# Kernel tuning notes

Measured on AMD Instinct MI355X. Metric: run time of the kernel, lower is better.

## Reference

```python
import jax, jax.numpy as jnp
import numpy as np

B, S, D = 16, 2048, 400
HEADS, HEAD_SIZE = 4, 100
SCALE = 1.0 / np.float32(100.0 ** 0.5)


def setup_inputs() -> dict:
    key = jax.random.key(0)
    ks = jax.random.split(key, 8)
    return {
        "x": jax.random.normal(ks[0], (B, S, D), jnp.float32),
        "attn_kernel": jax.random.normal(ks[1], (3, D, HEAD_SIZE), jnp.float32) * 0.05,
        "attn_dense": jax.random.normal(ks[2], (D, HEADS * HEAD_SIZE), jnp.float32) * 0.05,
        "d1_w": jax.random.normal(ks[3], (400, 400), jnp.float32) * 0.05,
        "d1_b": jnp.zeros((400,), jnp.float32),
        "fc1_w": jax.random.normal(ks[4], (800, 512), jnp.float32) * 0.05,
        "fc1_b": jnp.zeros((512,), jnp.float32),
        "fc2_w": jax.random.normal(ks[5], (512, 256), jnp.float32) * 0.05,
        "fc2_b": jnp.zeros((256,), jnp.float32),
    }


def reference(x, attn_kernel, attn_dense, d1_w, d1_b, fc1_w, fc1_b, fc2_w, fc2_b):
    # Multi-head attention. NOTE: the original loops `heads` times over the SAME
    # shared kernel, so all 4 head outputs are identical; compute once, tile.
    WQ = jnp.einsum('bsd,dh->bsh', x, attn_kernel[0])  # [B,S,100]
    WK = jnp.einsum('bsd,dh->bsh', x, attn_kernel[1])
    WV = jnp.einsum('bsd,dh->bsh', x, attn_kernel[2])
    scores = jnp.einsum('bqh,bkh->bqk', WQ, WK) * SCALE  # [B,S,S]
    probs = jax.nn.softmax(scores, axis=-1)
    V = jnp.einsum('bqk,bkh->bqh', probs, WV)  # [B,S,100]
    out = jnp.tile(V, (1, 1, HEADS))  # concat of identical heads -> [B,S,400]
    out = jnp.einsum('bsd,de->bse', out, attn_dense)  # [B,S,400]
    # Dropout layers are identity at inference.
    h = jax.nn.relu(jnp.einsum('bsd,de->bse', out, d1_w) + d1_b)  # [B,S,400]
    pooled = jnp.concatenate([jnp.max(h, axis=1), jnp.mean(h, axis=1)], axis=-1)  # [B,800]
    h = jax.nn.relu(pooled @ fc1_w + fc1_b)  # [B,512]
    h = jax.nn.relu(h @ fc2_w + fc2_b)  # [B,256]
    return h
```

## Files before the change

kernel.cpp:

```cpp
#include <hip/hip_runtime.h>

typedef __attribute__((ext_vector_type(8))) _Float16 f16x8;
typedef __attribute__((ext_vector_type(4))) float f4v;
typedef __attribute__((ext_vector_type(8))) unsigned short us8;
typedef __attribute__((ext_vector_type(4))) unsigned short us4;
typedef unsigned short u16;

__device__ __forceinline__ u16 h2b(_Float16 h) { return __builtin_bit_cast(u16, h); }
__device__ __forceinline__ float b2f(u16 b) {
    return (float)__builtin_bit_cast(_Float16, b);
}

#define BAR() do { asm volatile("s_waitcnt lgkmcnt(0)" ::: "memory"); \
                   __builtin_amdgcn_s_barrier(); } while (0)

__global__ void k_w2p(const float* __restrict__ ad, const float* __restrict__ d1w,
                      float* __restrict__ w2p) {
    int i = blockIdx.x * 256 + threadIdx.x;
    if (i >= 51200) return;
    int es = blockIdx.y;
    int d = i / 400, j = i % 400;
    float acc = 0.f;
    if (d < 100) {
        const float* a0 = ad + d * 400 + es * 100;
        const float* wr = d1w + (es * 100) * 400 + j;
        #pragma unroll 4
        for (int e = 0; e < 100; ++e) {
            float av = a0[e] + a0[40000 + e] + a0[80000 + e] + a0[120000 + e];
            acc += av * wr[e * 400];
        }
    }
    w2p[es * 51200 + i] = acc;
}

__global__ void k_w2r(const float* __restrict__ w2p, u16* __restrict__ w2f) {
    int i = blockIdx.x * 256 + threadIdx.x;
    if (i >= 51200) return;
    float acc = w2p[i] + w2p[51200 + i] + w2p[102400 + i] + w2p[153600 + i];
    int d = i / 400, j = i % 400;
    int idx = ((j >> 4) * 4 + (d >> 5)) * 512 + (((d >> 3) & 3) * 16 + (j & 15)) * 8 + (d & 7);
    w2f[idx] = h2b((_Float16)acc);
}

__global__ void k_wprep(const float* __restrict__ ak, u16* __restrict__ wsp) {
    int i = blockIdx.x * 256 + threadIdx.x;
    if (i >= 159744) return;
    int k = i & 31, n = (i >> 5) & 127;
    int xx = i >> 12;
    int ks = xx % 13, m = xx / 13;
    int gk = ks * 32 + k;
    float v = (n < 100 && gk < 400) ? ak[m * 40000 + gk * 100 + n] : 0.f;
    _Float16 hb = (_Float16)v;
    _Float16 lb = (_Float16)(v - (float)hb);
    long base = (long)xx * 8192;
    int pos = n * 32 + ((((k >> 3) ^ (n & 3)) << 3) | (k & 7));
    wsp[base + pos] = h2b(hb);
    wsp[base + 4096 + pos] = h2b(lb);
}

__global__ __launch_bounds__(512) void k_gemm_qkv(
    const float* __restrict__ x, const u16* __restrict__ wsp,
    u16* __restrict__ QH, u16* __restrict__ KH, u16* __restrict__ VT) {
    __shared__ __align__(16) u16 smem[32768];

    const int tid = threadIdx.x;
    const int bx = blockIdx.x;
    const int m = bx % 3;
    const int rowblk = bx / 3;
    const long row0 = (long)rowblk * 128;
    const int w = tid >> 6, l = tid & 63, g = l >> 4, c15 = l & 15;
    const int sr = tid >> 2, skc = tid & 3;

    f4v acc[8];
    #pragma unroll
    for (int nt = 0; nt < 8; ++nt) acc[nt] = (f4v){0.f, 0.f, 0.f, 0.f};

    const u16* wbase = wsp + (long)m * 13 * 8192;
    float4 xr0, xr1;
    us8 wr[2];
    const int xpos = sr * 32 + ((skc * 8) ^ ((sr & 3) << 3));

    {
        const float* xp = x + (row0 + sr) * 400 + skc * 8;
        xr0 = *(const float4*)xp;
        xr1 = *(const float4*)(xp + 4);
        #pragma unroll
        for (int r = 0; r < 2; ++r)
            wr[r] = *(const us8*)&wbase[(long)(tid + r * 512) * 8];
        float va[8] = {xr0.x, xr0.y, xr0.z, xr0.w, xr1.x, xr1.y, xr1.z, xr1.w};
        us8 hi8, lo8;
        #pragma unroll
        for (int j = 0; j < 8; ++j) {
            _Float16 h = (_Float16)va[j];
            hi8[j] = h2b(h);
            lo8[j] = h2b((_Float16)(va[j] - (float)h));
        }
        *(us8*)&smem[xpos] = hi8;
        *(us8*)&smem[4096 + xpos] = lo8;
        #pragma unroll
        for (int r = 0; r < 2; ++r) {
            int u = tid + r * 512;
            *(us8*)&smem[8192 + (u >> 9) * 4096 + (u & 511) * 8] = wr[r];
        }
        const float* xp1 = x + (row0 + sr) * 400 + 32 + skc * 8;
        xr0 = *(const float4*)xp1;
        xr1 = *(const float4*)(xp1 + 4);
        const u16* wsrc = wbase + 8192;
        #pragma unroll
        for (int r = 0; r < 2; ++r)
            wr[r] = *(const us8*)&wsrc[(long)(tid + r * 512) * 8];
    }

    for (int ks = 0; ks < 13; ++ks) {
        BAR();
        u16* cb = smem + (ks & 1) * 16384;
        u16* sb = smem + ((ks & 1) ^ 1) * 16384;
        if (ks + 1 < 13) {
            float va[8] = {xr0.x, xr0.y, xr0.z, xr0.w, xr1.x, xr1.y, xr1.z, xr1.w};
            us8 hi8, lo8;
            #pragma unroll
            for (int j = 0; j < 8; ++j) {
                _Float16 h = (_Float16)va[j];
                hi8[j] = h2b(h);
                lo8[j] = h2b((_Float16)(va[j] - (float)h));
            }
            *(us8*)&sb[xpos] = hi8;
            *(us8*)&sb[4096 + xpos] = lo8;
            #pragma unroll
            for (int r = 0; r < 2; ++r) {
                int u = tid + r * 512;
                *(us8*)&sb[8192 + (u >> 9) * 4096 + (u & 511) * 8] = wr[r];
            }
            if (ks + 2 < 13) {
                if ((ks + 2) * 32 + skc * 8 < 400) {
                    const float* xp = x + (row0 + sr) * 400 + (ks + 2) * 32 + skc * 8;
                    xr0 = *(const float4*)xp;
                    xr1 = *(const float4*)(xp + 4);
                } else {
                    xr0 = make_float4(0.f, 0.f, 0.f, 0.f);
                    xr1 = make_float4(0.f, 0.f, 0.f, 0.f);
                }
                const u16* wsrc = wbase + (long)(ks + 2) * 8192;
                #pragma unroll
                for (int r = 0; r < 2; ++r)
                    wr[r] = *(const us8*)&wsrc[(long)(tid + r * 512) * 8];
            }
        }
        const int arow = w * 16 + c15;
        const int axo = arow * 32 + ((g * 8) ^ ((arow & 3) << 3));
        f16x8 ah = *(const f16x8*)&cb[axo];
        f16x8 al = *(const f16x8*)&cb[4096 + axo];
        __builtin_amdgcn_s_setprio(1);
        #pragma unroll
        for (int nt = 0; nt < 8; ++nt) {
            int brow = nt * 16 + c15;
            int boff = brow * 32 + ((g * 8) ^ ((brow & 3) << 3));
            f16x8 bh = *(const f16x8*)&cb[8192 + boff];
            acc[nt] = __builtin_amdgcn_mfma_f32_16x16x32_f16(ah, bh, acc[nt], 0, 0, 0);
            acc[nt] = __builtin_amdgcn_mfma_f32_16x16x32_f16(al, bh, acc[nt], 0, 0, 0);
            if (m != 2) {
                f16x8 bl = *(const f16x8*)&cb[12288 + boff];
                acc[nt] = __builtin_amdgcn_mfma_f32_16x16x32_f16(ah, bl, acc[nt], 0, 0, 0);
            }
        }
        __builtin_amdgcn_s_setprio(0);
    }
    BAR();
    u16* epi = smem;

    if (m == 2) {
        const int q0 = w * 16 + 4 * g;
        const int vtile = q0 >> 6, q0w = q0 & 63;
        #pragma unroll
        for (int nt = 0; nt < 8; ++nt) {
            int d = nt * 16 + c15;
            if (d < 112) {
                us4 v4;
                #pragma unroll
                for (int r = 0; r < 4; ++r) v4[r] = h2b((_Float16)acc[nt][r]);
                *(us4*)&epi[vtile * 8192 + d * 64 + (q0w ^ ((d & 7) << 3))] = v4;
            }
        }
        __syncthreads();
        #pragma unroll
        for (int r = 0; r < 4; ++r) {
            int u = tid + r * 512;
            int vt2 = u >> 10, uu = u & 1023;
            if (uu < 896)
                *(us8*)&VT[((long)(2 * rowblk + vt2)) * 8192 + (long)uu * 8] =
                    *(const us8*)&epi[u * 8];
        }
    } else {
        const float qs = (m == 0) ? 0.14426950408889634f : 1.0f;
        #pragma unroll
        for (int nt = 0; nt < 8; ++nt) {
            #pragma unroll
            for (int r = 0; r < 4; ++r) {
                int row = w * 16 + 4 * g + r, col = nt * 16 + c15;
                epi[row * 128 + (col ^ ((row & 7) << 3))] =
                    h2b((_Float16)(acc[nt][r] * qs));
            }
        }
        __syncthreads();
        if (m == 0) {
            #pragma unroll
            for (int r = 0; r < 4; ++r) {
                int u = tid + r * 512;
                int row = u >> 4, c = u & 15;
                *(us8*)&QH[(row0 + row) * 128 + c * 8] =
                    *(const us8*)&epi[row * 128 + ((c * 8) ^ ((row & 7) << 3))];
            }
        } else {
            u16* dst = KH + (long)rowblk * 16384;
            #pragma unroll
            for (int r = 0; r < 4; ++r) {
                int u = tid + r * 512;
                *(us8*)&dst[(long)u * 8] = *(const us8*)&epi[u * 8];
            }
        }
    }
}

__global__ __launch_bounds__(512) void k_flash(
    const u16* __restrict__ Qg, const u16* __restrict__ Kg,
    const u16* __restrict__ Vg, u16* __restrict__ VOI,
    float* __restrict__ ML) {
    __shared__ __align__(16) char KS[2][16384];
    __shared__ __align__(16) char VS[2][14336];
    __shared__ __align__(16) char PS[8][2048];

    const int tid = threadIdx.x;
    const int w = tid >> 6, l = tid & 63, g = l >> 4, c15 = l & 15;
    const int b = blockIdx.y, qt = blockIdx.x, half = blockIdx.z;
    const int t0 = half * 16;

    const u16* qp = Qg + ((long)b * 2048 + qt * 128 + w * 16 + c15) * 128;
    f16x8 qh[4];
    #pragma unroll
    for (int ks = 0; ks < 4; ++ks) qh[ks] = *(const f16x8*)(qp + ks * 32 + g * 8);

    f4v O[7];
    #pragma unroll
    for (int i = 0; i < 7; ++i) O[i] = (f4v){0.f, 0.f, 0.f, 0.f};
    float lrow = 0.f;

    const u16* Kb = Kg + (long)b * 32 * 8192;
    const u16* Vb = Vg + (long)b * 32 * 8192;
    char* Pw = PS[w];

    us8 kreg[2], vreg[2];
    #pragma unroll
    for (int r = 0; r < 2; ++r) {
        int u = tid + r * 512;
        kreg[r] = *(const us8*)(Kb + (long)t0 * 8192 + (long)u * 8);
        if (u < 896) vreg[r] = *(const us8*)(Vb + (long)t0 * 8192 + (long)u * 8);
    }
    #pragma unroll
    for (int r = 0; r < 2; ++r) {
        int u = tid + r * 512;
        *(us8*)(KS[0] + u * 16) = kreg[r];
        if (u < 896) *(us8*)(VS[0] + u * 16) = vreg[r];
    }
    #pragma unroll
    for (int r = 0; r < 2; ++r) {
        int u = tid + r * 512;
        kreg[r] = *(const us8*)(Kb + (long)(t0 + 1) * 8192 + (long)u * 8);
        if (u < 896) vreg[r] = *(const us8*)(Vb + (long)(t0 + 1) * 8192 + (long)u * 8);
    }

    for (int t = t0; t < t0 + 16; ++t) {
        const int cur = (t - t0) & 1;
        BAR();
        if (t + 1 < t0 + 16) {
            #pragma unroll
            for (int r = 0; r < 2; ++r) {
                int u = tid + r * 512;
                *(us8*)(KS[cur ^ 1] + u * 16) = kreg[r];
                if (u < 896) *(us8*)(VS[cur ^ 1] + u * 16) = vreg[r];
            }
            if (t + 2 < t0 + 16) {
                #pragma unroll
                for (int r = 0; r < 2; ++r) {
                    int u = tid + r * 512;
                    kreg[r] = *(const us8*)(Kb + (long)(t + 2) * 8192 + (long)u * 8);
                    if (u < 896)
                        vreg[r] = *(const us8*)(Vb + (long)(t + 2) * 8192 + (long)u * 8);
                }
            }
        }
        const char* Kc = KS[cur];
        const char* Vc = VS[cur];

        f4v s[4];
        #pragma unroll
        for (int nt = 0; nt < 4; ++nt) s[nt] = (f4v){0.f, 0.f, 0.f, 0.f};
        __builtin_amdgcn_s_setprio(1);
        #pragma unroll
        for (int ks = 0; ks < 4; ++ks) {
            #pragma unroll
            for (int nt = 0; nt < 4; ++nt) {
                int key = nt * 16 + c15;
                f16x8 kf = *(const f16x8*)(Kc + key * 256 +
                                           ((ks * 64 + g * 16) ^ ((key & 7) << 4)));
                s[nt] = __builtin_amdgcn_mfma_f32_16x16x32_f16(kf, qh[ks], s[nt], 0, 0, 0);
            }
        }
        __builtin_amdgcn_s_setprio(0);

        float sum = 0.f;
        #pragma unroll
        for (int nt = 0; nt < 4; ++nt) {
            #pragma unroll
            for (int r = 0; r < 4; ++r) {
                float p = exp2f(s[nt][r]);
                s[nt][r] = p;
                sum += p;
            }
        }
        sum += __shfl_xor(sum, 16);
        sum += __shfl_xor(sum, 32);
        lrow += sum;

        #pragma unroll
        for (int nt = 0; nt < 4; ++nt) {
            uint2 pw2;
            pw2.x = __builtin_bit_cast(unsigned int,
                        __builtin_amdgcn_cvt_pkrtz(s[nt][0], s[nt][1]));
            pw2.y = __builtin_bit_cast(unsigned int,
                        __builtin_amdgcn_cvt_pkrtz(s[nt][2], s[nt][3]));
            *(uint2*)(Pw + c15 * 128 + ((32 * nt + 8 * g) ^ ((c15 & 7) << 4))) = pw2;
        }
        __builtin_amdgcn_s_setprio(1);
        #pragma unroll
        for (int k0 = 0; k0 < 2; ++k0) {
            f16x8 pa = *(const f16x8*)(Pw + c15 * 128 +
                                       ((k0 * 64 + g * 16) ^ ((c15 & 7) << 4)));
            #pragma unroll
            for (int dt = 0; dt < 7; ++dt) {
                int d = dt * 16 + c15;
                f16x8 vf = *(const f16x8*)(Vc + d * 128 +
                                           ((k0 * 64 + g * 16) ^ ((d & 7) << 4)));
                O[dt] = __builtin_amdgcn_mfma_f32_16x16x32_f16(pa, vf, O[dt], 0, 0, 0);
            }
        }
        __builtin_amdgcn_s_setprio(0);
    }

    if (g == 0) {
        ((float*)Pw)[c15] = lrow;
        ML[half * 32768 + b * 2048 + qt * 128 + w * 16 + c15] = lrow;
    }
    float linv[4];
    #pragma unroll
    for (int r = 0; r < 4; ++r) linv[r] = 1.f / ((float*)Pw)[4 * g + r];
    u16* vout = VOI + (long)half * 4194304 + ((long)b * 16 + qt) * 16384;
    #pragma unroll
    for (int r = 0; r < 4; ++r) {
        int rowl = w * 16 + 4 * g + r;
        int rsw = (4 * g + r) & 7;
        #pragma unroll
        for (int dt = 0; dt < 7; ++dt) {
            int d = dt * 16 + c15;
            int pos = rowl * 128 + ((((d >> 3) ^ rsw) << 3) | (d & 7));
            vout[pos] = h2b((_Float16)(O[dt][r] * linv[r]));
        }
    }
}

__global__ __launch_bounds__(256) void k_hpool(
    const u16* __restrict__ VOI, const float* __restrict__ ML,
    const u16* __restrict__ W2F, const float* __restrict__ d1b,
    float* __restrict__ pmax, float* __restrict__ psum) {
    __shared__ __align__(16) u16 A[8192];
    __shared__ float redM[4][400], redS[4][400];
    __shared__ float wgt[64][2];
    const int tid = threadIdx.x;
    const int w = tid >> 6, l = tid & 63, g = l >> 4, c15 = l & 15;
    const int b = blockIdx.y, rt = blockIdx.x;

    if (tid < 64) {
        float a = ML[b * 2048 + rt * 64 + tid];
        float c = ML[32768 + b * 2048 + rt * 64 + tid];
        float inv = 1.f / (a + c);
        wgt[tid][0] = a * inv;
        wgt[tid][1] = c * inv;
    }
    __syncthreads();

    const u16* s1 = VOI + ((long)b * 32 + rt) * 8192;
    const u16* s2 = s1 + 4194304;
    #pragma unroll
    for (int r = 0; r < 4; ++r) {
        int u = tid + r * 256;
        int row = u >> 4;
        us8 p1 = *(const us8*)&s1[(long)u * 8];
        us8 p2 = *(const us8*)&s2[(long)u * 8];
        float w1 = wgt[row][0], w2 = wgt[row][1];
        us8 o;
        #pragma unroll
        for (int j = 0; j < 8; ++j)
            o[j] = h2b((_Float16)(w1 * b2f(p1[j]) + w2 * b2f(p2[j])));
        *(us8*)&A[u * 8] = o;
    }
    __syncthreads();

    const int arow = w * 16 + c15;
    f16x8 af[4];
    #pragma unroll
    for (int ks = 0; ks < 4; ++ks)
        af[ks] = *(const f16x8*)&A[arow * 128 + ((ks * 32 + g * 8) ^ ((arow & 7) << 3))];

    for (int nt = 0; nt < 25; ++nt) {
        f4v acc = (f4v){0.f, 0.f, 0.f, 0.f};
        #pragma unroll
        for (int ks = 0; ks < 4; ++ks) {
            f16x8 bf = *(const f16x8*)&W2F[(nt * 4 + ks) * 512 + l * 8];
            acc = __builtin_amdgcn_mfma_f32_16x16x32_f16(af[ks], bf, acc, 0, 0, 0);
        }
        float bias = d1b[nt * 16 + c15];
        float mx4 = -1e30f, sm4 = 0.f;
        #pragma unroll
        for (int r = 0; r < 4; ++r) {
            float h = fmaxf(acc[r] + bias, 0.f);
            mx4 = fmaxf(mx4, h);
            sm4 += h;
        }
        mx4 = fmaxf(mx4, __shfl_xor(mx4, 16));
        mx4 = fmaxf(mx4, __shfl_xor(mx4, 32));
        sm4 += __shfl_xor(sm4, 16);
        sm4 += __shfl_xor(sm4, 32);
        if (g == 0) {
            redM[w][nt * 16 + c15] = mx4;
            redS[w][nt * 16 + c15] = sm4;
        }
    }
    __syncthreads();
    for (int j = tid; j < 400; j += 256) {
        float mx = fmaxf(fmaxf(redM[0][j], redM[1][j]), fmaxf(redM[2][j], redM[3][j]));
        float sm = redS[0][j] + redS[1][j] + redS[2][j] + redS[3][j];
        pmax[((long)b * 32 + rt) * 400 + j] = mx;
        psum[((long)b * 32 + rt) * 400 + j] = sm;
    }
}

__global__ __launch_bounds__(256) void k_pred(
    const float* __restrict__ pmax, const float* __restrict__ psum,
    float* __restrict__ pooled) {
    __shared__ float rm[16][17], rs[16][17];
    const int b = blockIdx.x, jt = blockIdx.y, tid = threadIdx.x;
    const int jo = tid & 15, ts = tid >> 4;
    const int j = jt * 16 + jo;
    float mx = -1e30f, sm = 0.f;
    for (int t = ts; t < 32; t += 16) {
        mx = fmaxf(mx, pmax[((long)b * 32 + t) * 400 + j]);
        sm += psum[((long)b * 32 + t) * 400 + j];
    }
    rm[ts][jo] = mx; rs[ts][jo] = sm;
    __syncthreads();
    if (tid < 16) {
        float m2 = rm[0][tid], s2 = rs[0][tid];
        #pragma unroll
        for (int t = 1; t < 16; ++t) { m2 = fmaxf(m2, rm[t][tid]); s2 += rs[t][tid]; }
        pooled[b * 800 + jt * 16 + tid] = m2;
        pooled[b * 800 + 400 + jt * 16 + tid] = s2 * (1.f / 2048.f);
    }
}

__global__ __launch_bounds__(256) void k_fc1(
    const float* __restrict__ pooled, const float* __restrict__ w,
    const float* __restrict__ bias, float* __restrict__ out) {
    __shared__ float pl[800];
    __shared__ float red[16][17];
    const int b = blockIdx.x, jt = blockIdx.y, tid = threadIdx.x;
    const int jo = tid & 15, ks = tid >> 4;
    const int j = jt * 16 + jo;
    for (int i = tid; i < 800; i += 256) pl[i] = pooled[b * 800 + i];
    __syncthreads();
    float acc = 0.f;
    #pragma unroll 5
    for (int kk = 0; kk < 50; ++kk) {
        int k = ks * 50 + kk;
        acc += pl[k] * w[k * 512 + j];
    }
    red[ks][jo] = acc;
    __syncthreads();
    if (tid < 16) {
        float s = red[0][tid];
        #pragma unroll
        for (int t = 1; t < 16; ++t) s += red[t][tid];
        out[b * 512 + jt * 16 + tid] = fmaxf(s + bias[jt * 16 + tid], 0.f);
    }
}

__global__ __launch_bounds__(256) void k_fc2(
    const float* __restrict__ h, const float* __restrict__ w,
    const float* __restrict__ bias, float* __restrict__ out) {
    __shared__ float hl[512];
    __shared__ float red[16][17];
    const int b = blockIdx.x, jt = blockIdx.y, tid = threadIdx.x;
    const int jo = tid & 15, ks = tid >> 4;
    const int j = jt * 16 + jo;
    for (int i = tid; i < 512; i += 256) hl[i] = h[b * 512 + i];
    __syncthreads();
    float acc = 0.f;
    #pragma unroll 4
    for (int kk = 0; kk < 32; ++kk) {
        int k = ks * 32 + kk;
        acc += hl[k] * w[k * 256 + j];
    }
    red[ks][jo] = acc;
    __syncthreads();
    if (tid < 16) {
        float s = red[0][tid];
        #pragma unroll
        for (int t = 1; t < 16; ++t) s += red[t][tid];
        out[b * 256 + jt * 16 + tid] = fmaxf(s + bias[jt * 16 + tid], 0.f);
    }
}

extern "C" void kernel_launch(void* const* d_in, const int* in_sizes, int n_in,
                              void* d_out, int out_size, void* d_ws, size_t ws_size,
                              hipStream_t stream) {
    const float* x          = (const float*)d_in[0];
    const float* attn_kernel= (const float*)d_in[1];
    const float* attn_dense = (const float*)d_in[2];
    const float* d1_w       = (const float*)d_in[3];
    const float* d1_b       = (const float*)d_in[4];
    const float* fc1_w      = (const float*)d_in[5];
    const float* fc1_b      = (const float*)d_in[6];
    const float* fc2_w      = (const float*)d_in[7];
    const float* fc2_b      = (const float*)d_in[8];
    float* out = (float*)d_out;
    char*  wsb = (char*)d_ws;

    u16*    QH   = (u16*)(wsb);
    u16*    KH   = (u16*)(wsb + 8388608);
    u16*    VT   = (u16*)(wsb + 16777216);
    u16*    VOI  = (u16*)(wsb + 25165824);
    u16*    WSP  = (u16*)(wsb + 41943040);
    u16*    W2F  = (u16*)(wsb + 42582016);
    float*  PMAX = (float*)(wsb + 42844416);
    float*  PSUM = (float*)(wsb + 43663616);
    float*  ML   = (float*)(wsb + 44566784);
    float*  W2P  = (float*)(wsb + 44828928);
    float*  POOL = (float*)(wsb + 45648128);
    float*  FC1  = (float*)(wsb + 45699328);

    k_wprep<<<624, 256, 0, stream>>>(attn_kernel, WSP);
    k_w2p <<<dim3(200, 4), 256, 0, stream>>>(attn_dense, d1_w, W2P);
    k_w2r <<<200, 256, 0, stream>>>(W2P, W2F);
    k_gemm_qkv<<<768, 512, 0, stream>>>(x, WSP, QH, KH, VT);
    k_flash<<<dim3(16, 16, 2), 512, 0, stream>>>(QH, KH, VT, VOI, ML);
    k_hpool<<<dim3(32, 16), 256, 0, stream>>>(VOI, ML, W2F, d1_b, PMAX, PSUM);
    k_pred<<<dim3(16, 25), 256, 0, stream>>>(PMAX, PSUM, POOL);
    k_fc1 <<<dim3(16, 32), 256, 0, stream>>>(POOL, fc1_w, fc1_b, FC1);
    k_fc2 <<<dim3(16, 16), 256, 0, stream>>>(FC1, fc2_w, fc2_b, out);
}
```

Before: 153.0 us.

## Fuse Q/K/V projections into one block and double query rows per flash wave

The QKV GEMM now computes Q, K and V for a 128-row tile in a single block, so each x tile is loaded and hi/lo split once instead of three times. The grid shrinks from 768 to 256 blocks and shared memory grows to 96KB. The flash kernel halves its threads to 256 and has each wave process 32 query rows, reusing every K/V fragment read from LDS for two MFMAs. The trade-off is higher register pressure, fewer waves per block, and less occupancy and parallelism in both kernels.

```diff
diff --git a/kernel.cpp b/kernel.cpp
--- a/kernel.cpp
+++ b/kernel.cpp
@@ -61,32 +61,39 @@
 __global__ __launch_bounds__(512) void k_gemm_qkv(
     const float* __restrict__ x, const u16* __restrict__ wsp,
     u16* __restrict__ QH, u16* __restrict__ KH, u16* __restrict__ VT) {
-    __shared__ __align__(16) u16 smem[32768];
+    __shared__ __align__(16) u16 smem[49152];
 
     const int tid = threadIdx.x;
-    const int bx = blockIdx.x;
-    const int m = bx % 3;
-    const int rowblk = bx / 3;
+    const int rowblk = blockIdx.x;
     const long row0 = (long)rowblk * 128;
     const int w = tid >> 6, l = tid & 63, g = l >> 4, c15 = l & 15;
     const int sr = tid >> 2, skc = tid & 3;
 
-    f4v acc[8];
-    #pragma unroll
-    for (int nt = 0; nt < 8; ++nt) acc[nt] = (f4v){0.f, 0.f, 0.f, 0.f};
-
-    const u16* wbase = wsp + (long)m * 13 * 8192;
+    f4v aQ[8], aK[8], aV[8];
+    #pragma unroll
+    for (int nt = 0; nt < 8; ++nt) {
+        aQ[nt] = (f4v){0.f, 0.f, 0.f, 0.f};
+        aK[nt] = (f4v){0.f, 0.f, 0.f, 0.f};
+        aV[nt] = (f4v){0.f, 0.f, 0.f, 0.f};
+    }
+
+    const u16* wq  = wsp;
+    const u16* wkh = wsp + 106496;
+    const u16* wkl = wsp + 110592;
+    const u16* wv  = wsp + 212992;
+
     float4 xr0, xr1;
-    us8 wr[2];
+    us8 wr[4];
     const int xpos = sr * 32 + ((skc * 8) ^ ((sr & 3) << 3));
 
     {
         const float* xp = x + (row0 + sr) * 400 + skc * 8;
         xr0 = *(const float4*)xp;
         xr1 = *(const float4*)(xp + 4);
-        #pragma unroll
-        for (int r = 0; r < 2; ++r)
-            wr[r] = *(const us8*)&wbase[(long)(tid + r * 512) * 8];
+        wr[0] = *(const us8*)&wq [(long)tid * 8];
+        wr[1] = *(const us8*)&wkh[(long)tid * 8];
+        wr[2] = *(const us8*)&wkl[(long)tid * 8];
+        wr[3] = *(const us8*)&wv [(long)tid * 8];
         float va[8] = {xr0.x, xr0.y, xr0.z, xr0.w, xr1.x, xr1.y, xr1.z, xr1.w};
         us8 hi8, lo8;
         #pragma unroll
@@ -97,24 +104,23 @@
         }
         *(us8*)&smem[xpos] = hi8;
         *(us8*)&smem[4096 + xpos] = lo8;
-        #pragma unroll
-        for (int r = 0; r < 2; ++r) {
-            int u = tid + r * 512;
-            *(us8*)&smem[8192 + (u >> 9) * 4096 + (u & 511) * 8] = wr[r];
-        }
+        *(us8*)&smem[8192  + tid * 8] = wr[0];
+        *(us8*)&smem[12288 + tid * 8] = wr[1];
+        *(us8*)&smem[16384 + tid * 8] = wr[2];
+        *(us8*)&smem[20480 + tid * 8] = wr[3];
         const float* xp1 = x + (row0 + sr) * 400 + 32 + skc * 8;
         xr0 = *(const float4*)xp1;
         xr1 = *(const float4*)(xp1 + 4);
-        const u16* wsrc = wbase + 8192;
-        #pragma unroll
-        for (int r = 0; r < 2; ++r)
-            wr[r] = *(const us8*)&wsrc[(long)(tid + r * 512) * 8];
+        wr[0] = *(const us8*)&wq [8192 + (long)tid * 8];
+        wr[1] = *(const us8*)&wkh[8192 + (long)tid * 8];
+        wr[2] = *(const us8*)&wkl[8192 + (long)tid * 8];
+        wr[3] = *(const us8*)&wv [8192 + (long)tid * 8];
     }
 
     for (int ks = 0; ks < 13; ++ks) {
         BAR();
-        u16* cb = smem + (ks & 1) * 16384;
-        u16* sb = smem + ((ks & 1) ^ 1) * 16384;
+        u16* cb = smem + (ks & 1) * 24576;
+        u16* sb = smem + ((ks & 1) ^ 1) * 24576;
         if (ks + 1 < 13) {
             float va[8] = {xr0.x, xr0.y, xr0.z, xr0.w, xr1.x, xr1.y, xr1.z, xr1.w};
             us8 hi8, lo8;
@@ -126,11 +132,10 @@
             }
             *(us8*)&sb[xpos] = hi8;
             *(us8*)&sb[4096 + xpos] = lo8;
-            #pragma unroll
-            for (int r = 0; r < 2; ++r) {
-                int u = tid + r * 512;
-                *(us8*)&sb[8192 + (u >> 9) * 4096 + (u & 511) * 8] = wr[r];
-            }
+            *(us8*)&sb[8192  + tid * 8] = wr[0];
+            *(us8*)&sb[12288 + tid * 8] = wr[1];
+            *(us8*)&sb[16384 + tid * 8] = wr[2];
+            *(us8*)&sb[20480 + tid * 8] = wr[3];
             if (ks + 2 < 13) {
                 if ((ks + 2) * 32 + skc * 8 < 400) {
                     const float* xp = x + (row0 + sr) * 400 + (ks + 2) * 32 + skc * 8;
@@ -140,10 +145,11 @@
                     xr0 = make_float4(0.f, 0.f, 0.f, 0.f);
                     xr1 = make_float4(0.f, 0.f, 0.f, 0.f);
                 }
-                const u16* wsrc = wbase + (long)(ks + 2) * 8192;
-                #pragma unroll
-                for (int r = 0; r < 2; ++r)
-                    wr[r] = *(const us8*)&wsrc[(long)(tid + r * 512) * 8];
+                long wo = (long)(ks + 2) * 8192 + (long)tid * 8;
+                wr[0] = *(const us8*)&wq [wo];
+                wr[1] = *(const us8*)&wkh[wo];
+                wr[2] = *(const us8*)&wkl[wo];
+                wr[3] = *(const us8*)&wv [wo];
             }
         }
         const int arow = w * 16 + c15;
@@ -155,20 +161,63 @@
         for (int nt = 0; nt < 8; ++nt) {
             int brow = nt * 16 + c15;
             int boff = brow * 32 + ((g * 8) ^ ((brow & 3) << 3));
-            f16x8 bh = *(const f16x8*)&cb[8192 + boff];
-            acc[nt] = __builtin_amdgcn_mfma_f32_16x16x32_f16(ah, bh, acc[nt], 0, 0, 0);
-            acc[nt] = __builtin_amdgcn_mfma_f32_16x16x32_f16(al, bh, acc[nt], 0, 0, 0);
-            if (m != 2) {
-                f16x8 bl = *(const f16x8*)&cb[12288 + boff];
-                acc[nt] = __builtin_amdgcn_mfma_f32_16x16x32_f16(ah, bl, acc[nt], 0, 0, 0);
-            }
+            f16x8 qb = *(const f16x8*)&cb[8192 + boff];
+            aQ[nt] = __builtin_amdgcn_mfma_f32_16x16x32_f16(ah, qb, aQ[nt], 0, 0, 0);
+            aQ[nt] = __builtin_amdgcn_mfma_f32_16x16x32_f16(al, qb, aQ[nt], 0, 0, 0);
+            f16x8 kh = *(const f16x8*)&cb[12288 + boff];
+            aK[nt] = __builtin_amdgcn_mfma_f32_16x16x32_f16(ah, kh, aK[nt], 0, 0, 0);
+            aK[nt] = __builtin_amdgcn_mfma_f32_16x16x32_f16(al, kh, aK[nt], 0, 0, 0);
+            f16x8 kl = *(const f16x8*)&cb[16384 + boff];
+            aK[nt] = __builtin_amdgcn_mfma_f32_16x16x32_f16(ah, kl, aK[nt], 0, 0, 0);
+            f16x8 vb = *(const f16x8*)&cb[20480 + boff];
+            aV[nt] = __builtin_amdgcn_mfma_f32_16x16x32_f16(ah, vb, aV[nt], 0, 0, 0);
+            aV[nt] = __builtin_amdgcn_mfma_f32_16x16x32_f16(al, vb, aV[nt], 0, 0, 0);
         }
         __builtin_amdgcn_s_setprio(0);
     }
     BAR();
     u16* epi = smem;
 
-    if (m == 2) {
+    {
+        const float qs = 0.14426950408889634f;
+        #pragma unroll
+        for (int nt = 0; nt < 8; ++nt) {
+            #pragma unroll
+            for (int r = 0; r < 4; ++r) {
+                int row = w * 16 + 4 * g + r, col = nt * 16 + c15;
+                epi[row * 128 + (col ^ ((row & 7) << 3))] =
+                    h2b((_Float16)(aQ[nt][r] * qs));
+            }
+        }
+        __syncthreads();
+        #pragma unroll
+        for (int r = 0; r < 4; ++r) {
+            int u = tid + r * 512;
+            int row = u >> 4, c = u & 15;
+            *(us8*)&QH[(row0 + row) * 128 + c * 8] =
+                *(const us8*)&epi[row * 128 + ((c * 8) ^ ((row & 7) << 3))];
+        }
+        __syncthreads();
+    }
+    {
+        #pragma unroll
+        for (int nt = 0; nt < 8; ++nt) {
+            #pragma unroll
+            for (int r = 0; r < 4; ++r) {
+                int row = w * 16 + 4 * g + r, col = nt * 16 + c15;
+                epi[row * 128 + (col ^ ((row & 7) << 3))] = h2b((_Float16)aK[nt][r]);
+            }
+        }
+        __syncthreads();
+        u16* dst = KH + (long)rowblk * 16384;
+        #pragma unroll
+        for (int r = 0; r < 4; ++r) {
+            int u = tid + r * 512;
+            *(us8*)&dst[(long)u * 8] = *(const us8*)&epi[u * 8];
+        }
+        __syncthreads();
+    }
+    {
         const int q0 = w * 16 + 4 * g;
         const int vtile = q0 >> 6, q0w = q0 & 63;
         #pragma unroll
@@ -177,7 +226,7 @@
             if (d < 112) {
                 us4 v4;
                 #pragma unroll
-                for (int r = 0; r < 4; ++r) v4[r] = h2b((_Float16)acc[nt][r]);
+                for (int r = 0; r < 4; ++r) v4[r] = h2b((_Float16)aV[nt][r]);
                 *(us4*)&epi[vtile * 8192 + d * 64 + (q0w ^ ((d & 7) << 3))] = v4;
             }
         }
@@ -190,80 +239,57 @@
                 *(us8*)&VT[((long)(2 * rowblk + vt2)) * 8192 + (long)uu * 8] =
                     *(const us8*)&epi[u * 8];
         }
-    } else {
-        const float qs = (m == 0) ? 0.14426950408889634f : 1.0f;
-        #pragma unroll
-        for (int nt = 0; nt < 8; ++nt) {
-            #pragma unroll
-            for (int r = 0; r < 4; ++r) {
-                int row = w * 16 + 4 * g + r, col = nt * 16 + c15;
-                epi[row * 128 + (col ^ ((row & 7) << 3))] =
-                    h2b((_Float16)(acc[nt][r] * qs));
-            }
-        }
-        __syncthreads();
-        if (m == 0) {
-            #pragma unroll
-            for (int r = 0; r < 4; ++r) {
-                int u = tid + r * 512;
-                int row = u >> 4, c = u & 15;
-                *(us8*)&QH[(row0 + row) * 128 + c * 8] =
-                    *(const us8*)&epi[row * 128 + ((c * 8) ^ ((row & 7) << 3))];
-            }
-        } else {
-            u16* dst = KH + (long)rowblk * 16384;
-            #pragma unroll
-            for (int r = 0; r < 4; ++r) {
-                int u = tid + r * 512;
-                *(us8*)&dst[(long)u * 8] = *(const us8*)&epi[u * 8];
-            }
-        }
-    }
-}
-
-__global__ __launch_bounds__(512) void k_flash(
+    }
+}
+
+__global__ __launch_bounds__(256) void k_flash(
     const u16* __restrict__ Qg, const u16* __restrict__ Kg,
     const u16* __restrict__ Vg, u16* __restrict__ VOI,
     float* __restrict__ ML) {
     __shared__ __align__(16) char KS[2][16384];
     __shared__ __align__(16) char VS[2][14336];
-    __shared__ __align__(16) char PS[8][2048];
+    __shared__ __align__(16) char PS[4][4096];
 
     const int tid = threadIdx.x;
     const int w = tid >> 6, l = tid & 63, g = l >> 4, c15 = l & 15;
     const int b = blockIdx.y, qt = blockIdx.x, half = blockIdx.z;
     const int t0 = half * 16;
 
-    const u16* qp = Qg + ((long)b * 2048 + qt * 128 + w * 16 + c15) * 128;
-    f16x8 qh[4];
-    #pragma unroll
-    for (int ks = 0; ks < 4; ++ks) qh[ks] = *(const f16x8*)(qp + ks * 32 + g * 8);
-
-    f4v O[7];
-    #pragma unroll
-    for (int i = 0; i < 7; ++i) O[i] = (f4v){0.f, 0.f, 0.f, 0.f};
-    float lrow = 0.f;
+    const u16* qp = Qg + ((long)b * 2048 + qt * 128 + w * 32 + c15) * 128;
+    f16x8 qh[2][4];
+    #pragma unroll
+    for (int h = 0; h < 2; ++h)
+        #pragma unroll
+        for (int ks = 0; ks < 4; ++ks)
+            qh[h][ks] = *(const f16x8*)(qp + h * 2048 + ks * 32 + g * 8);
+
+    f4v O[2][7];
+    #pragma unroll
+    for (int h = 0; h < 2; ++h)
+        #pragma unroll
+        for (int i = 0; i < 7; ++i) O[h][i] = (f4v){0.f, 0.f, 0.f, 0.f};
+    float lrow[2] = {0.f, 0.f};
 
     const u16* Kb = Kg + (long)b * 32 * 8192;
     const u16* Vb = Vg + (long)b * 32 * 8192;
     char* Pw = PS[w];
 
-    us8 kreg[2], vreg[2];
-    #pragma unroll
-    for (int r = 0; r < 2; ++r) {
-        int u = tid + r * 512;
+    us8 kreg[4], vreg[4];
+    #pragma unroll
+    for (int r = 0; r < 4; ++r) {
+        int u = tid + r * 256;
         kreg[r] = *(const us8*)(Kb + (long)t0 * 8192 + (long)u * 8);
         if (u < 896) vreg[r] = *(const us8*)(Vb + (long)t0 * 8192 + (long)u * 8);
     }
     #pragma unroll
-    for (int r = 0; r < 2; ++r) {
-        int u = tid + r * 512;
+    for (int r = 0; r < 4; ++r) {
+        int u = tid + r * 256;
         *(us8*)(KS[0] + u * 16) = kreg[r];
         if (u < 896) *(us8*)(VS[0] + u * 16) = vreg[r];
     }
     #pragma unroll
-    for (int r = 0; r < 2; ++r) {
-        int u = tid + r * 512;
+    for (int r = 0; r < 4; ++r) {
+        int u = tid + r * 256;
         kreg[r] = *(const us8*)(Kb + (long)(t0 + 1) * 8192 + (long)u * 8);
         if (u < 896) vreg[r] = *(const us8*)(Vb + (long)(t0 + 1) * 8192 + (long)u * 8);
     }
@@ -273,15 +299,15 @@
         BAR();
         if (t + 1 < t0 + 16) {
             #pragma unroll
-            for (int r = 0; r < 2; ++r) {
-                int u = tid + r * 512;
+            for (int r = 0; r < 4; ++r) {
+                int u = tid + r * 256;
                 *(us8*)(KS[cur ^ 1] + u * 16) = kreg[r];
                 if (u < 896) *(us8*)(VS[cur ^ 1] + u * 16) = vreg[r];
             }
             if (t + 2 < t0 + 16) {
                 #pragma unroll
-                for (int r = 0; r < 2; ++r) {
-                    int u = tid + r * 512;
+                for (int r = 0; r < 4; ++r) {
+                    int u = tid + r * 256;
                     kreg[r] = *(const us8*)(Kb + (long)(t + 2) * 8192 + (long)u * 8);
                     if (u < 896)
                         vreg[r] = *(const us8*)(Vb + (long)(t + 2) * 8192 + (long)u * 8);
@@ -291,9 +317,11 @@
         const char* Kc = KS[cur];
         const char* Vc = VS[cur];
 
-        f4v s[4];
-        #pragma unroll
-        for (int nt = 0; nt < 4; ++nt) s[nt] = (f4v){0.f, 0.f, 0.f, 0.f};
+        f4v s[2][4];
+        #pragma unroll
+        for (int h = 0; h < 2; ++h)
+            #pragma unroll
+            for (int nt = 0; nt < 4; ++nt) s[h][nt] = (f4v){0.f, 0.f, 0.f, 0.f};
         __builtin_amdgcn_s_setprio(1);
         #pragma unroll
         for (int ks = 0; ks < 4; ++ks) {
@@ -302,67 +330,86 @@
                 int key = nt * 16 + c15;
                 f16x8 kf = *(const f16x8*)(Kc + key * 256 +
                                            ((ks * 64 + g * 16) ^ ((key & 7) << 4)));
-                s[nt] = __builtin_amdgcn_mfma_f32_16x16x32_f16(kf, qh[ks], s[nt], 0, 0, 0);
+                s[0][nt] = __builtin_amdgcn_mfma_f32_16x16x32_f16(kf, qh[0][ks], s[0][nt], 0, 0, 0);
+                s[1][nt] = __builtin_amdgcn_mfma_f32_16x16x32_f16(kf, qh[1][ks], s[1][nt], 0, 0, 0);
             }
         }
         __builtin_amdgcn_s_setprio(0);
 
-        float sum = 0.f;
-        #pragma unroll
-        for (int nt = 0; nt < 4; ++nt) {
-            #pragma unroll
-            for (int r = 0; r < 4; ++r) {
-                float p = exp2f(s[nt][r]);
-                s[nt][r] = p;
-                sum += p;
-            }
-        }
-        sum += __shfl_xor(sum, 16);
-        sum += __shfl_xor(sum, 32);
-        lrow += sum;
-
-        #pragma unroll
-        for (int nt = 0; nt < 4; ++nt) {
-            uint2 pw2;
-            pw2.x = __builtin_bit_cast(unsigned int,
-                        __builtin_amdgcn_cvt_pkrtz(s[nt][0], s[nt][1]));
-            pw2.y = __builtin_bit_cast(unsigned int,
-                        __builtin_amdgcn_cvt_pkrtz(s[nt][2], s[nt][3]));
-            *(uint2*)(Pw + c15 * 128 + ((32 * nt + 8 * g) ^ ((c15 & 7) << 4))) = pw2;
+        #pragma unroll
+        for (int h = 0; h < 2; ++h) {
+            float sum = 0.f;
+            #pragma unroll
+            for (int nt = 0; nt < 4; ++nt) {
+                #pragma unroll
+                for (int r = 0; r < 4; ++r) {
+                    float p = exp2f(s[h][nt][r]);
+                    s[h][nt][r] = p;
+                    sum += p;
+                }
+            }
+            sum += __shfl_xor(sum, 16);
+            sum += __shfl_xor(sum, 32);
+            lrow[h] += sum;
+        }
+
+        #pragma unroll
+        for (int h = 0; h < 2; ++h) {
+            #pragma unroll
+            for (int nt = 0; nt < 4; ++nt) {
+                uint2 pw2;
+                pw2.x = __builtin_bit_cast(unsigned int,
+                            __builtin_amdgcn_cvt_pkrtz(s[h][nt][0], s[h][nt][1]));
+                pw2.y = __builtin_bit_cast(unsigned int,
+                            __builtin_amdgcn_cvt_pkrtz(s[h][nt][2], s[h][nt][3]));
+                *(uint2*)(Pw + (h * 16 + c15) * 128 +
+                          ((32 * nt + 8 * g) ^ ((c15 & 7) << 4))) = pw2;
+            }
         }
         __builtin_amdgcn_s_setprio(1);
         #pragma unroll
         for (int k0 = 0; k0 < 2; ++k0) {
-            f16x8 pa = *(const f16x8*)(Pw + c15 * 128 +
-                                       ((k0 * 64 + g * 16) ^ ((c15 & 7) << 4)));
+            f16x8 pa0 = *(const f16x8*)(Pw + c15 * 128 +
+                                        ((k0 * 64 + g * 16) ^ ((c15 & 7) << 4)));
+            f16x8 pa1 = *(const f16x8*)(Pw + (16 + c15) * 128 +
+                                        ((k0 * 64 + g * 16) ^ ((c15 & 7) << 4)));
             #pragma unroll
             for (int dt = 0; dt < 7; ++dt) {
                 int d = dt * 16 + c15;
                 f16x8 vf = *(const f16x8*)(Vc + d * 128 +
                                            ((k0 * 64 + g * 16) ^ ((d & 7) << 4)));
-                O[dt] = __builtin_amdgcn_mfma_f32_16x16x32_f16(pa, vf, O[dt], 0, 0, 0);
+                O[0][dt] = __builtin_amdgcn_mfma_f32_16x16x32_f16(pa0, vf, O[0][dt], 0, 0, 0);
+                O[1][dt] = __builtin_amdgcn_mfma_f32_16x16x32_f16(pa1, vf, O[1][dt], 0, 0, 0);
             }
         }
         __builtin_amdgcn_s_setprio(0);
     }
 
     if (g == 0) {
-        ((float*)Pw)[c15] = lrow;
-        ML[half * 32768 + b * 2048 + qt * 128 + w * 16 + c15] = lrow;
-    }
-    float linv[4];
-    #pragma unroll
-    for (int r = 0; r < 4; ++r) linv[r] = 1.f / ((float*)Pw)[4 * g + r];
+        ((float*)Pw)[c15] = lrow[0];
+        ((float*)Pw)[16 + c15] = lrow[1];
+        ML[half * 32768 + b * 2048 + qt * 128 + w * 32 + c15] = lrow[0];
+        ML[half * 32768 + b * 2048 + qt * 128 + w * 32 + 16 + c15] = lrow[1];
+    }
+    float linv[2][4];
+    #pragma unroll
+    for (int h = 0; h < 2; ++h)
+        #pragma unroll
+        for (int r = 0; r < 4; ++r)
+            linv[h][r] = 1.f / ((float*)Pw)[h * 16 + 4 * g + r];
     u16* vout = VOI + (long)half * 4194304 + ((long)b * 16 + qt) * 16384;
     #pragma unroll
-    for (int r = 0; r < 4; ++r) {
-        int rowl = w * 16 + 4 * g + r;
-        int rsw = (4 * g + r) & 7;
-        #pragma unroll
-        for (int dt = 0; dt < 7; ++dt) {
-            int d = dt * 16 + c15;
-            int pos = rowl * 128 + ((((d >> 3) ^ rsw) << 3) | (d & 7));
-            vout[pos] = h2b((_Float16)(O[dt][r] * linv[r]));
+    for (int h = 0; h < 2; ++h) {
+        #pragma unroll
+        for (int r = 0; r < 4; ++r) {
+            int rowl = w * 32 + h * 16 + 4 * g + r;
+            int rsw = (4 * g + r) & 7;
+            #pragma unroll
+            for (int dt = 0; dt < 7; ++dt) {
+                int d = dt * 16 + c15;
+                int pos = rowl * 128 + ((((d >> 3) ^ rsw) << 3) | (d & 7));
+                vout[pos] = h2b((_Float16)(O[h][dt][r] * linv[h][r]));
+            }
         }
     }
 }
@@ -549,8 +596,8 @@
     k_wprep<<<624, 256, 0, stream>>>(attn_kernel, WSP);
     k_w2p <<<dim3(200, 4), 256, 0, stream>>>(attn_dense, d1_w, W2P);
     k_w2r <<<200, 256, 0, stream>>>(W2P, W2F);
-    k_gemm_qkv<<<768, 512, 0, stream>>>(x, WSP, QH, KH, VT);
-    k_flash<<<dim3(16, 16, 2), 512, 0, stream>>>(QH, KH, VT, VOI, ML);
+    k_gemm_qkv<<<256, 512, 0, stream>>>(x, WSP, QH, KH, VT);
+    k_flash<<<dim3(16, 16, 2), 256, 0, stream>>>(QH, KH, VT, VOI, ML);
     k_hpool<<<dim3(32, 16), 256, 0, stream>>>(VOI, ML, W2F, d1_b, PMAX, PSUM);
     k_pred<<<dim3(16, 25), 256, 0, stream>>>(PMAX, PSUM, POOL);
     k_fc1 <<<dim3(16, 32), 256, 0, stream>>>(POOL, fc1_w, fc1_b, FC1);
```

Result: faster. 137.1 us (-10.3%).
